# Kernel tuning notes

Hardware: AMD Instinct MI355X
Metric: run time of the kernel (lower is better)

## Reference

```python
import jax, jax.numpy as jnp
import numpy as np

N_HEADS = 16

def setup_inputs() -> dict:
    key = jax.random.key(0)
    ks = jax.random.split(key, 6)
    B, H, F, P, D = 2048, 1024, 4096, 512, 1024
    x = jax.random.normal(ks[0], (B, H), dtype=jnp.float32)
    # module inits features/prototypes ~ U(-0.27, 1)
    features = jax.random.uniform(ks[1], (F, D), minval=-0.27, maxval=1.0, dtype=jnp.float32)
    prototypes = jax.random.uniform(ks[2], (P, D), minval=-0.27, maxval=1.0, dtype=jnp.float32)
    # theta/alpha/beta are zero-init in the module; use small random values so output is non-trivial
    theta = jax.random.normal(ks[3], (N_HEADS, 1), dtype=jnp.float32)
    alpha = jax.random.normal(ks[4], (N_HEADS, 1), dtype=jnp.float32)
    beta = jax.random.normal(ks[5], (N_HEADS, 1), dtype=jnp.float32)
    return {"x": x, "features": features, "prototypes": prototypes,
            "theta": theta, "alpha": alpha, "beta": beta}

def reference(x, features, prototypes, theta, alpha, beta):
    n_heads = N_HEADS
    B, total_dim = x.shape
    d = total_dim // n_heads
    xh = x.reshape(B, n_heads, d)                       # b h d
    fh = features.reshape(-1, n_heads, d).transpose(1, 0, 2)    # h f d
    ph = prototypes.reshape(-1, n_heads, d).transpose(1, 0, 2)  # h p d
    x_features = jnp.einsum('bhd,hfd->bhf', xh, fh)     # [B,h,F]
    p_features = jnp.einsum('hpd,hfd->hpf', ph, fh)     # [h,P,F]
    x_present = jax.nn.relu(x_features)
    p_present = jax.nn.relu(p_features)
    x_weighted = x_features * x_present
    p_weighted = p_features * p_present
    # head-batched GEMMs sharing operands
    common = jnp.einsum('bhf,hpf->bhp', x_weighted, p_weighted)
    x_p_interaction = jnp.einsum('bhf,hpf->bhp', x_weighted, p_present)
    p_x_interaction = jnp.einsum('bhf,hpf->bhp', x_present, p_weighted)
    x_weighted_sum = x_weighted.sum(axis=2, keepdims=True)      # [B,h,1]
    p_weighted_sum = p_weighted.sum(axis=2)[None, :, :]         # [1,h,P]
    x_distinctive = x_weighted_sum - x_p_interaction
    p_distinctive = p_weighted_sum - p_x_interaction
    th = theta.reshape(1, n_heads, 1)
    al = alpha.reshape(1, n_heads, 1)
    be = beta.reshape(1, n_heads, 1)
    out = th * common - al * x_distinctive - be * p_distinctive  # [B,h,P]
    return out.reshape(B, -1)
```

## Files before the change

### kernel.cpp

```cpp
#include <hip/hip_runtime.h>
#include <cstdint>

#define NH 16
#define DH 64
#define FF 4096
#define PP 512
#define BB 2048

typedef __bf16 bf16x8 __attribute__((ext_vector_type(8)));
typedef float f32x4 __attribute__((ext_vector_type(4)));
typedef float fl4 __attribute__((ext_vector_type(4)));
typedef unsigned short us4 __attribute__((ext_vector_type(4)));
typedef unsigned int u32x2 __attribute__((ext_vector_type(2)));

__device__ __forceinline__ unsigned short f2bf(float f) {
  unsigned u = __float_as_uint(f);
  u += 0x7FFFu + ((u >> 16) & 1u);
  return (unsigned short)(u >> 16);
}

__device__ __forceinline__ unsigned int pkbf(float lo, float hi) {
  unsigned a = __float_as_uint(lo) + 0x8000u;
  unsigned b = __float_as_uint(hi) + 0x8000u;
  return __builtin_amdgcn_perm(b, a, 0x07060302u);
}

__device__ __forceinline__ void gload_lds16(const void* g, void* l) {
  __builtin_amdgcn_global_load_lds(
      (const __attribute__((address_space(1))) void*)g,
      (__attribute__((address_space(3))) void*)(unsigned int)(unsigned long long)l,
      16, 0, 0);
}

__global__ void cvt_bf16(const float* __restrict__ src,
                         unsigned short* __restrict__ dst, int n4) {
  int i = blockIdx.x * blockDim.x + threadIdx.x;
  if (i >= n4) return;
  fl4 v = ((const fl4*)src)[i];
  us4 o;
  o.x = f2bf(v.x); o.y = f2bf(v.y); o.z = f2bf(v.z); o.w = f2bf(v.w);
  ((us4*)dst)[i] = o;
}

__global__ __launch_bounds__(256, 2) void gemm_proto(
    const unsigned short* __restrict__ Abf, const unsigned short* __restrict__ Fbf,
    unsigned short* __restrict__ O1, unsigned short* __restrict__ O2,
    float* __restrict__ pws,
    const float* __restrict__ theta, const float* __restrict__ alpha,
    const float* __restrict__ beta) {
  const int h = blockIdx.z;
  const int n0 = blockIdx.x * 128;
  const int lm0 = blockIdx.y * 128;
  const int t = threadIdx.x;

  __shared__ __align__(16) char As[128 * 128];
  __shared__ __align__(16) char Bs[128 * 128];

  {
    const char* ab = (const char*)(Abf + (size_t)lm0 * 1024 + h * 64);
    const char* bb = (const char*)(Fbf + (size_t)n0 * 1024 + h * 64);
#pragma unroll
    for (int r = 0; r < 4; ++r) {
      int o = r * 4096 + t * 16;
      int row = o >> 7, col = o & 127;
      gload_lds16(ab + (size_t)row * 2048 + col, As + o);
      gload_lds16(bb + (size_t)row * 2048 + col, Bs + o);
    }
  }
  __syncthreads();

  const int wave = t >> 6, lane = t & 63;
  const int wm = wave & 1, wn = wave >> 1;
  const int quad = lane >> 4, lr = lane & 15;

  f32x4 acc[4][4];
#pragma unroll
  for (int i = 0; i < 4; ++i)
#pragma unroll
    for (int j = 0; j < 4; ++j) acc[i][j] = (f32x4){0.f, 0.f, 0.f, 0.f};

#pragma unroll
  for (int s = 0; s < 2; ++s) {
    bf16x8 av[4], bv[4];
#pragma unroll
    for (int fm = 0; fm < 4; ++fm) {
      int row = wm * 64 + fm * 16 + lr;
      av[fm] = *(const bf16x8*)(As + row * 128 + s * 64 + quad * 16);
    }
#pragma unroll
    for (int fn = 0; fn < 4; ++fn) {
      int row = wn * 64 + fn * 16 + lr;
      bv[fn] = *(const bf16x8*)(Bs + row * 128 + s * 64 + quad * 16);
    }
#pragma unroll
    for (int fm = 0; fm < 4; ++fm)
#pragma unroll
      for (int fn = 0; fn < 4; ++fn)
        acc[fm][fn] = __builtin_amdgcn_mfma_f32_16x16x32_bf16(av[fm], bv[fn],
                                                              acc[fm][fn], 0, 0, 0);
  }

  const float th = theta[h], al = alpha[h], be = beta[h];

#pragma unroll
  for (int fm = 0; fm < 4; ++fm) {
    int prow = lm0 + wm * 64 + fm * 16 + quad * 4;
    float rs0 = 0.f, rs1 = 0.f, rs2 = 0.f, rs3 = 0.f;
#pragma unroll
    for (int fn = 0; fn < 4; ++fn) {
      int f = n0 + wn * 64 + fn * 16 + lr;
#pragma unroll
      for (int i = 0; i < 4; ++i) {
        float pf = acc[fm][fn][i];
        float pp = fmaxf(pf, 0.f);
        float pw = pf * pp;
        size_t idx = ((size_t)(h * PP + prow + i)) * FF + f;
        O1[idx] = f2bf(th * pw + al * pp - al);
        O2[idx] = f2bf(be * pw);
        if (i == 0) rs0 += pw;
        else if (i == 1) rs1 += pw;
        else if (i == 2) rs2 += pw;
        else rs3 += pw;
      }
    }
    float rs[4] = {rs0, rs1, rs2, rs3};
#pragma unroll
    for (int i = 0; i < 4; ++i) {
      float s = rs[i];
      s += __shfl_xor(s, 1);
      s += __shfl_xor(s, 2);
      s += __shfl_xor(s, 4);
      s += __shfl_xor(s, 8);
      if (lr == 0) atomicAdd(&pws[h * PP + prow + i], be * s);
    }
  }
}

__global__ __launch_bounds__(256, 2) void fused_main(
    const unsigned short* __restrict__ x_bf, const unsigned short* __restrict__ f_bf,
    const unsigned short* __restrict__ Q1, const unsigned short* __restrict__ Q2,
    const float* __restrict__ pws, float* __restrict__ out) {
  const int h = blockIdx.z;
  const int n0 = blockIdx.x * 256;
  const int m0 = blockIdx.y * 128;
  const int t = threadIdx.x;
  const int wave = t >> 6, lane = t & 63;
  const int wm = wave & 1, wn = wave >> 1;
  const int quad = lane >> 4, lr = lane & 15;
  const int key8 = lr & 7;
  const int key2 = (lr >> 1) & 3;

  __shared__ __align__(16) char sF[4096];
  __shared__ __align__(16) char sQ1[16384];
  __shared__ __align__(16) char sQ2[16384];
  __shared__ __align__(16) char sXw[8192];
  __shared__ __align__(16) char sXp[8192];

  bf16x8 xh[2][2];
#pragma unroll
  for (int bn = 0; bn < 2; ++bn)
#pragma unroll
    for (int s = 0; s < 2; ++s) {
      int b = m0 + wave * 32 + bn * 16 + lr;
      xh[bn][s] = *(const bf16x8*)(x_bf + (size_t)b * 1024 + h * 64 + s * 32 + quad * 8);
    }

  int af_off[2][2];
#pragma unroll
  for (int fm = 0; fm < 2; ++fm)
#pragma unroll
    for (int s = 0; s < 2; ++s)
      af_off[fm][s] = (fm * 16 + lr) * 128 + (((s * 4 + quad) ^ key8) * 16);

  int cw_off[2][2];
#pragma unroll
  for (int fm = 0; fm < 2; ++fm)
#pragma unroll
    for (int bn = 0; bn < 2; ++bn)
      cw_off[fm][bn] = (wave * 32 + bn * 16 + lr) * 64 +
                       (((fm * 2 + (quad >> 1)) ^ key2) * 16) + (quad & 1) * 8;

  int aw_off[4];
#pragma unroll
  for (int fm = 0; fm < 4; ++fm)
    aw_off[fm] = (wm * 64 + fm * 16 + lr) * 64 + ((quad ^ key2) * 16);

  int bq_off[8];
#pragma unroll
  for (int fn = 0; fn < 8; ++fn)
    bq_off[fn] = (wn * 128 + fn * 16 + lr) * 64 + ((quad ^ key2) * 16);

  const char* srcF;
  {
    int row = t >> 3, c = t & 7, cs = c ^ (row & 7);
    srcF = (const char*)f_bf + h * 128 + (size_t)row * 2048 + cs * 16;
  }
  const char* srcQ1[4];
  const char* srcQ2[4];
  {
    const char* q1b = (const char*)(Q1 + ((size_t)h * PP + n0) * FF);
    const char* q2b = (const char*)(Q2 + ((size_t)h * PP + n0) * FF);
#pragma unroll
    for (int r = 0; r < 4; ++r) {
      int ci = r * 256 + t, row = ci >> 2, c = ci & 3, cs = c ^ ((row >> 1) & 3);
      srcQ1[r] = q1b + (size_t)row * 8192 + cs * 16;
      srcQ2[r] = q2b + (size_t)row * 8192 + cs * 16;
    }
  }

  f32x4 acc[4][8];
#pragma unroll
  for (int i = 0; i < 4; ++i)
#pragma unroll
    for (int j = 0; j < 8; ++j) acc[i][j] = (f32x4){0.f, 0.f, 0.f, 0.f};

  for (int it = 0; it < FF / 32; ++it) {
    __syncthreads();
    gload_lds16(srcF, sF + t * 16);
    srcF += 32 * 2048;
#pragma unroll
    for (int r = 0; r < 4; ++r) {
      gload_lds16(srcQ1[r], sQ1 + r * 4096 + t * 16);
      gload_lds16(srcQ2[r], sQ2 + r * 4096 + t * 16);
      srcQ1[r] += 64;
      srcQ2[r] += 64;
    }
    __syncthreads();

    f32x4 xf[2][2];
#pragma unroll
    for (int fm = 0; fm < 2; ++fm)
#pragma unroll
      for (int bn = 0; bn < 2; ++bn) xf[fm][bn] = (f32x4){0.f, 0.f, 0.f, 0.f};
#pragma unroll
    for (int s = 0; s < 2; ++s)
#pragma unroll
      for (int fm = 0; fm < 2; ++fm) {
        bf16x8 af = *(const bf16x8*)(sF + af_off[fm][s]);
#pragma unroll
        for (int bn = 0; bn < 2; ++bn)
          xf[fm][bn] = __builtin_amdgcn_mfma_f32_16x16x32_bf16(af, xh[bn][s],
                                                               xf[fm][bn], 0, 0, 0);
      }

#pragma unroll
    for (int fm = 0; fm < 2; ++fm)
#pragma unroll
      for (int bn = 0; bn < 2; ++bn) {
        float v0 = xf[fm][bn][0], v1 = xf[fm][bn][1];
        float v2 = xf[fm][bn][2], v3 = xf[fm][bn][3];
        float p0 = fmaxf(v0, 0.f), p1 = fmaxf(v1, 0.f);
        float p2 = fmaxf(v2, 0.f), p3 = fmaxf(v3, 0.f);
        u32x2 w, p;
        w.x = pkbf(v0 * p0, v1 * p1);
        w.y = pkbf(v2 * p2, v3 * p3);
        p.x = pkbf(p0, p1);
        p.y = pkbf(p2, p3);
        *(u32x2*)(sXw + cw_off[fm][bn]) = w;
        *(u32x2*)(sXp + cw_off[fm][bn]) = p;
      }
    __syncthreads();

    bf16x8 aw[4], ap[4];
#pragma unroll
    for (int fm = 0; fm < 4; ++fm) {
      aw[fm] = *(const bf16x8*)(sXw + aw_off[fm]);
      ap[fm] = *(const bf16x8*)(sXp + aw_off[fm]);
    }
#pragma unroll
    for (int fn = 0; fn < 8; ++fn) {
      bf16x8 b1 = *(const bf16x8*)(sQ1 + bq_off[fn]);
      bf16x8 b2 = *(const bf16x8*)(sQ2 + bq_off[fn]);
#pragma unroll
      for (int fm = 0; fm < 4; ++fm) {
        acc[fm][fn] = __builtin_amdgcn_mfma_f32_16x16x32_bf16(aw[fm], b1,
                                                              acc[fm][fn], 0, 0, 0);
        acc[fm][fn] = __builtin_amdgcn_mfma_f32_16x16x32_bf16(ap[fm], b2,
                                                              acc[fm][fn], 0, 0, 0);
      }
    }
  }

#pragma unroll
  for (int fn = 0; fn < 8; ++fn) {
    int p = n0 + wn * 128 + fn * 16 + lr;
    float sub = pws[h * PP + p];
#pragma unroll
    for (int fm = 0; fm < 4; ++fm) {
      int brow = m0 + wm * 64 + fm * 16 + quad * 4;
#pragma unroll
      for (int i = 0; i < 4; ++i) {
        out[(size_t)(brow + i) * (NH * PP) + h * PP + p] = acc[fm][fn][i] - sub;
      }
    }
  }
}

extern "C" void kernel_launch(void* const* d_in, const int* in_sizes, int n_in,
                              void* d_out, int out_size, void* d_ws, size_t ws_size,
                              hipStream_t stream) {
  const float* x = (const float*)d_in[0];
  const float* features = (const float*)d_in[1];
  const float* prototypes = (const float*)d_in[2];
  const float* theta = (const float*)d_in[3];
  const float* alpha = (const float*)d_in[4];
  const float* beta = (const float*)d_in[5];
  float* out = (float*)d_out;

  char* ws = (char*)d_ws;
  size_t off = 0;
  auto carve = [&](size_t bytes) -> char* {
    char* p = ws + off;
    off += (bytes + 255) & ~(size_t)255;
    return p;
  };
  unsigned short* x_bf = (unsigned short*)carve((size_t)BB * 1024 * 2);
  unsigned short* f_bf = (unsigned short*)carve((size_t)FF * 1024 * 2);
  unsigned short* p_bf = (unsigned short*)carve((size_t)PP * 1024 * 2);
  unsigned short* Q1 = (unsigned short*)carve((size_t)NH * PP * FF * 2);
  unsigned short* Q2 = (unsigned short*)carve((size_t)NH * PP * FF * 2);
  float* pws = (float*)carve((size_t)NH * PP * 4);

  cvt_bf16<<<2048, 256, 0, stream>>>(x, x_bf, BB * 1024 / 4);
  cvt_bf16<<<4096, 256, 0, stream>>>(features, f_bf, FF * 1024 / 4);
  cvt_bf16<<<512, 256, 0, stream>>>(prototypes, p_bf, PP * 1024 / 4);
  hipMemsetAsync(pws, 0, (size_t)NH * PP * 4, stream);

  gemm_proto<<<dim3(FF / 128, PP / 128, NH), 256, 0, stream>>>(
      p_bf, f_bf, Q1, Q2, pws, theta, alpha, beta);

  fused_main<<<dim3(PP / 256, BB / 128, NH), 256, 0, stream>>>(
      x_bf, f_bf, Q1, Q2, pws, out);
}
```

Before: 423.3 us.

## Shrink fused_main batch tile to 64 rows and merge conversion kernels

The main fused kernel now tiles 64 batch rows instead of 128. Each wave covers all 64 rows and 64 prototype columns, so the accumulator drops from 4x8 to 4x4 tiles, and occupancy rises to 3 blocks per CU. The grid doubles, so the Q1/Q2 prototype tiles and feature tiles are streamed twice as often, which raises global and L2 traffic per output. The three bf16 conversion launches are also merged into one kernel to save launch overhead.

```diff
diff --git a/kernel.cpp b/kernel.cpp
--- a/kernel.cpp
+++ b/kernel.cpp
@@ -32,14 +32,31 @@
       16, 0, 0);
 }
 
-__global__ void cvt_bf16(const float* __restrict__ src,
-                         unsigned short* __restrict__ dst, int n4) {
+__global__ void cvt_all(const float* __restrict__ x, const float* __restrict__ f,
+                        const float* __restrict__ p,
+                        unsigned short* __restrict__ xb,
+                        unsigned short* __restrict__ fb,
+                        unsigned short* __restrict__ pb) {
+  const int nx = BB * 1024 / 4, nf = FF * 1024 / 4, np = PP * 1024 / 4;
   int i = blockIdx.x * blockDim.x + threadIdx.x;
-  if (i >= n4) return;
-  fl4 v = ((const fl4*)src)[i];
+  const fl4* src;
+  us4* dst;
+  if (i < nx) {
+    src = (const fl4*)x + i;
+    dst = (us4*)xb + i;
+  } else if (i < nx + nf) {
+    src = (const fl4*)f + (i - nx);
+    dst = (us4*)fb + (i - nx);
+  } else if (i < nx + nf + np) {
+    src = (const fl4*)p + (i - nx - nf);
+    dst = (us4*)pb + (i - nx - nf);
+  } else {
+    return;
+  }
+  fl4 v = *src;
   us4 o;
   o.x = f2bf(v.x); o.y = f2bf(v.y); o.z = f2bf(v.z); o.w = f2bf(v.w);
-  ((us4*)dst)[i] = o;
+  *dst = o;
 }
 
 __global__ __launch_bounds__(256, 2) void gemm_proto(
@@ -136,16 +153,15 @@
   }
 }
 
-__global__ __launch_bounds__(256, 2) void fused_main(
+__global__ __launch_bounds__(256, 3) void fused_main(
     const unsigned short* __restrict__ x_bf, const unsigned short* __restrict__ f_bf,
     const unsigned short* __restrict__ Q1, const unsigned short* __restrict__ Q2,
     const float* __restrict__ pws, float* __restrict__ out) {
   const int h = blockIdx.z;
   const int n0 = blockIdx.x * 256;
-  const int m0 = blockIdx.y * 128;
+  const int m0 = blockIdx.y * 64;
   const int t = threadIdx.x;
   const int wave = t >> 6, lane = t & 63;
-  const int wm = wave & 1, wn = wave >> 1;
   const int quad = lane >> 4, lr = lane & 15;
   const int key8 = lr & 7;
   const int key2 = (lr >> 1) & 3;
@@ -153,17 +169,15 @@
   __shared__ __align__(16) char sF[4096];
   __shared__ __align__(16) char sQ1[16384];
   __shared__ __align__(16) char sQ2[16384];
-  __shared__ __align__(16) char sXw[8192];
-  __shared__ __align__(16) char sXp[8192];
-
-  bf16x8 xh[2][2];
-#pragma unroll
-  for (int bn = 0; bn < 2; ++bn)
-#pragma unroll
-    for (int s = 0; s < 2; ++s) {
-      int b = m0 + wave * 32 + bn * 16 + lr;
-      xh[bn][s] = *(const bf16x8*)(x_bf + (size_t)b * 1024 + h * 64 + s * 32 + quad * 8);
-    }
+  __shared__ __align__(16) char sXw[4096];
+  __shared__ __align__(16) char sXp[4096];
+
+  bf16x8 xh[2];
+#pragma unroll
+  for (int s = 0; s < 2; ++s) {
+    int b = m0 + wave * 16 + lr;
+    xh[s] = *(const bf16x8*)(x_bf + (size_t)b * 1024 + h * 64 + s * 32 + quad * 8);
+  }
 
   int af_off[2][2];
 #pragma unroll
@@ -172,23 +186,21 @@
     for (int s = 0; s < 2; ++s)
       af_off[fm][s] = (fm * 16 + lr) * 128 + (((s * 4 + quad) ^ key8) * 16);
 
-  int cw_off[2][2];
+  int cw_off[2];
 #pragma unroll
   for (int fm = 0; fm < 2; ++fm)
-#pragma unroll
-    for (int bn = 0; bn < 2; ++bn)
-      cw_off[fm][bn] = (wave * 32 + bn * 16 + lr) * 64 +
-                       (((fm * 2 + (quad >> 1)) ^ key2) * 16) + (quad & 1) * 8;
+    cw_off[fm] = (wave * 16 + lr) * 64 +
+                 (((fm * 2 + (quad >> 1)) ^ key2) * 16) + (quad & 1) * 8;
 
   int aw_off[4];
 #pragma unroll
   for (int fm = 0; fm < 4; ++fm)
-    aw_off[fm] = (wm * 64 + fm * 16 + lr) * 64 + ((quad ^ key2) * 16);
-
-  int bq_off[8];
-#pragma unroll
-  for (int fn = 0; fn < 8; ++fn)
-    bq_off[fn] = (wn * 128 + fn * 16 + lr) * 64 + ((quad ^ key2) * 16);
+    aw_off[fm] = (fm * 16 + lr) * 64 + ((quad ^ key2) * 16);
+
+  int bq_off[4];
+#pragma unroll
+  for (int fn = 0; fn < 4; ++fn)
+    bq_off[fn] = (wave * 64 + fn * 16 + lr) * 64 + ((quad ^ key2) * 16);
 
   const char* srcF;
   {
@@ -208,11 +220,11 @@
     }
   }
 
-  f32x4 acc[4][8];
+  f32x4 acc[4][4];
 #pragma unroll
   for (int i = 0; i < 4; ++i)
 #pragma unroll
-    for (int j = 0; j < 8; ++j) acc[i][j] = (f32x4){0.f, 0.f, 0.f, 0.f};
+    for (int j = 0; j < 4; ++j) acc[i][j] = (f32x4){0.f, 0.f, 0.f, 0.f};
 
   for (int it = 0; it < FF / 32; ++it) {
     __syncthreads();
@@ -227,38 +239,30 @@
     }
     __syncthreads();
 
-    f32x4 xf[2][2];
-#pragma unroll
-    for (int fm = 0; fm < 2; ++fm)
-#pragma unroll
-      for (int bn = 0; bn < 2; ++bn) xf[fm][bn] = (f32x4){0.f, 0.f, 0.f, 0.f};
+    f32x4 xf[2];
+    xf[0] = (f32x4){0.f, 0.f, 0.f, 0.f};
+    xf[1] = (f32x4){0.f, 0.f, 0.f, 0.f};
 #pragma unroll
     for (int s = 0; s < 2; ++s)
 #pragma unroll
       for (int fm = 0; fm < 2; ++fm) {
         bf16x8 af = *(const bf16x8*)(sF + af_off[fm][s]);
-#pragma unroll
-        for (int bn = 0; bn < 2; ++bn)
-          xf[fm][bn] = __builtin_amdgcn_mfma_f32_16x16x32_bf16(af, xh[bn][s],
-                                                               xf[fm][bn], 0, 0, 0);
+        xf[fm] = __builtin_amdgcn_mfma_f32_16x16x32_bf16(af, xh[s], xf[fm], 0, 0, 0);
       }
 
 #pragma unroll
-    for (int fm = 0; fm < 2; ++fm)
-#pragma unroll
-      for (int bn = 0; bn < 2; ++bn) {
-        float v0 = xf[fm][bn][0], v1 = xf[fm][bn][1];
-        float v2 = xf[fm][bn][2], v3 = xf[fm][bn][3];
-        float p0 = fmaxf(v0, 0.f), p1 = fmaxf(v1, 0.f);
-        float p2 = fmaxf(v2, 0.f), p3 = fmaxf(v3, 0.f);
-        u32x2 w, p;
-        w.x = pkbf(v0 * p0, v1 * p1);
-        w.y = pkbf(v2 * p2, v3 * p3);
-        p.x = pkbf(p0, p1);
-        p.y = pkbf(p2, p3);
-        *(u32x2*)(sXw + cw_off[fm][bn]) = w;
-        *(u32x2*)(sXp + cw_off[fm][bn]) = p;
-      }
+    for (int fm = 0; fm < 2; ++fm) {
+      float v0 = xf[fm][0], v1 = xf[fm][1], v2 = xf[fm][2], v3 = xf[fm][3];
+      float p0 = fmaxf(v0, 0.f), p1 = fmaxf(v1, 0.f);
+      float p2 = fmaxf(v2, 0.f), p3 = fmaxf(v3, 0.f);
+      u32x2 w, p;
+      w.x = pkbf(v0 * p0, v1 * p1);
+      w.y = pkbf(v2 * p2, v3 * p3);
+      p.x = pkbf(p0, p1);
+      p.y = pkbf(p2, p3);
+      *(u32x2*)(sXw + cw_off[fm]) = w;
+      *(u32x2*)(sXp + cw_off[fm]) = p;
+    }
     __syncthreads();
 
     bf16x8 aw[4], ap[4];
@@ -268,7 +272,7 @@
       ap[fm] = *(const bf16x8*)(sXp + aw_off[fm]);
     }
 #pragma unroll
-    for (int fn = 0; fn < 8; ++fn) {
+    for (int fn = 0; fn < 4; ++fn) {
       bf16x8 b1 = *(const bf16x8*)(sQ1 + bq_off[fn]);
       bf16x8 b2 = *(const bf16x8*)(sQ2 + bq_off[fn]);
 #pragma unroll
@@ -282,12 +286,12 @@
   }
 
 #pragma unroll
-  for (int fn = 0; fn < 8; ++fn) {
-    int p = n0 + wn * 128 + fn * 16 + lr;
+  for (int fn = 0; fn < 4; ++fn) {
+    int p = n0 + wave * 64 + fn * 16 + lr;
     float sub = pws[h * PP + p];
 #pragma unroll
     for (int fm = 0; fm < 4; ++fm) {
-      int brow = m0 + wm * 64 + fm * 16 + quad * 4;
+      int brow = m0 + fm * 16 + quad * 4;
 #pragma unroll
       for (int i = 0; i < 4; ++i) {
         out[(size_t)(brow + i) * (NH * PP) + h * PP + p] = acc[fm][fn][i] - sub;
@@ -321,14 +325,14 @@
   unsigned short* Q2 = (unsigned short*)carve((size_t)NH * PP * FF * 2);
   float* pws = (float*)carve((size_t)NH * PP * 4);
 
-  cvt_bf16<<<2048, 256, 0, stream>>>(x, x_bf, BB * 1024 / 4);
-  cvt_bf16<<<4096, 256, 0, stream>>>(features, f_bf, FF * 1024 / 4);
-  cvt_bf16<<<512, 256, 0, stream>>>(prototypes, p_bf, PP * 1024 / 4);
+  const int ncvt = (BB + FF + PP) * 1024 / 4;
+  cvt_all<<<(ncvt + 255) / 256, 256, 0, stream>>>(x, features, prototypes,
+                                                  x_bf, f_bf, p_bf);
   hipMemsetAsync(pws, 0, (size_t)NH * PP * 4, stream);
 
   gemm_proto<<<dim3(FF / 128, PP / 128, NH), 256, 0, stream>>>(
       p_bf, f_bf, Q1, Q2, pws, theta, alpha, beta);
 
-  fused_main<<<dim3(PP / 256, BB / 128, NH), 256, 0, stream>>>(
+  fused_main<<<dim3(PP / 256, BB / 64, NH), 256, 0, stream>>>(
       x_bf, f_bf, Q1, Q2, pws, out);
 }
```

Result: slower. 516.8 us (+22.1%).
